# Performance work log

Hardware: AMD Instinct MI355X
Metric: run time of the kernel (lower is better)

The kernel has to match this reference:

```python
import jax, jax.numpy as jnp
import numpy as np

B, C, H, W = 16, 256, 64, 64
OUT_C = 3
N_TOKENS = 512
N_RES = 3
RED = 4
CB = C // RED  # bottleneck channels in ResChain
DN = ('NCHW', 'OIHW', 'NCHW')


def _conv(x, w, pad):
    return jax.lax.conv_general_dilated(x, w, (1, 1), pad, dimension_numbers=DN)


def setup_inputs() -> dict:
    key = jax.random.key(0)
    ks = jax.random.split(key, 8)
    return {
        'input': jax.random.normal(ks[0], (B, C, H, W), jnp.float32),
        'embed': jax.random.normal(ks[1], (C, N_TOKENS), jnp.float32),  # Quantize codebook [dim, n_embed]
        'res_w1': jax.random.normal(ks[2], (N_RES, CB, C, 3, 3), jnp.float32) * 0.02,
        'res_b1': jnp.zeros((N_RES, CB), jnp.float32),
        'res_w2': jax.random.normal(ks[3], (N_RES, C, CB, 1, 1), jnp.float32) * 0.02,
        'res_b2': jnp.zeros((N_RES, C), jnp.float32),
        'out_w': jax.random.normal(ks[4], (OUT_C, C, 1, 1), jnp.float32) * 0.02,
        'out_b': jnp.zeros((OUT_C,), jnp.float32),
    }


def reference(input, embed, res_w1, res_b1, res_w2, res_b2, out_w, out_b):
    sg = jax.lax.stop_gradient
    # --- Quantize (VQ-VAE codebook lookup, straight-through) ---
    x = jnp.transpose(input, (0, 2, 3, 1))  # [B,H,W,C]
    flat = x.reshape(-1, C)                  # [N, C]
    # squared L2 distance to each code: ||f||^2 - 2 f.e + ||e||^2
    dist = (flat * flat).sum(-1, keepdims=True) - 2.0 * (flat @ embed) + (embed * embed).sum(0)
    idx = jnp.argmin(dist, axis=-1).reshape(B, H, W)        # [B,H,W] int
    quantize = jnp.take(embed.T, idx, axis=0)               # embed_code: [B,H,W,C]
    diff = jnp.mean((sg(quantize) - x) ** 2)
    quantize = x + sg(quantize - x)                         # straight-through
    q = jnp.transpose(quantize, (0, 3, 1, 2))               # [B,C,H,W]
    # --- dec: ResChain(n_res_block) + 1x1 conv ---
    for i in range(N_RES):
        h = jax.nn.relu(q)
        h = _conv(h, res_w1[i], 'SAME') + res_b1[i][None, :, None, None]
        h = jax.nn.relu(h)
        h = _conv(h, res_w2[i], 'VALID') + res_b2[i][None, :, None, None]
        q = q + h
    quant = _conv(q, out_w, 'VALID') + out_b[None, :, None, None]  # [B,OUT_C,H,W]
    # --- wordfreq: per-batch bincount over idx (no grad) ---
    flat_idx = idx.reshape(B, -1)
    seg = (flat_idx + jnp.arange(B, dtype=flat_idx.dtype)[:, None] * N_TOKENS).reshape(-1)
    counts = jax.ops.segment_sum(jnp.ones_like(seg, jnp.float32), seg, num_segments=B * N_TOKENS)
    wordfreq = counts.reshape(B, N_TOKENS) / float(H * W)
    return quant, diff.reshape(1), wordfreq
```

## Files before the change

### kernel.cpp

```cpp
#include <hip/hip_runtime.h>


typedef __attribute__((ext_vector_type(8))) short short8;
typedef __attribute__((ext_vector_type(16))) float f32x16;
typedef __attribute__((ext_vector_type(8))) _Float16 half8;
typedef __attribute__((ext_vector_type(2))) _Float16 half2_t;
typedef unsigned short ushort_t;
typedef unsigned long long u64;

#define WS_QA    0
#define WS_QB    8388608
#define WS_ET    16777216
#define WS_EN    16842752
#define WS_EPK   16843264
#define WS_W1PK  16908800
#define WS_W2PK  17129984
#define WS_DIFF  17154560
#define WS_TOK   17154568
#define WS_DST   17220104
#define WS_FN    17285640
#define WS_WL    17351176

#define MARGIN 0.12f

__device__ inline ushort_t f2bf(float f) {
  unsigned u = __float_as_uint(f);
  return (ushort_t)((u + 0x7fffu + ((u >> 16) & 1u)) >> 16);
}
__device__ inline float bf2f(ushort_t h) { return __uint_as_float(((unsigned)h) << 16); }
union HU { _Float16 h; ushort_t u; };
union S8H { short8 s; half8 h; half2_t h2[4]; };

__global__ __launch_bounds__(256) void prep_kernel(
    const float* __restrict__ embed, const float* __restrict__ w1,
    const float* __restrict__ w2, float* __restrict__ ws, float* __restrict__ wf) {
  int i = blockIdx.x * 256 + threadIdx.x;
  if (i < 131072) {
    int t = i >> 8, c = i & 255;
    ((ushort_t*)(ws + WS_ET))[i] = f2bf(embed[c * 512 + t]);
  }
  if (i < 512) {
    float s = 0.f;
    for (int c = 0; c < 256; ++c) { float v = embed[c * 512 + i]; s += v * v; }
    ws[WS_EN + i] = s;
  }
  if (i < 131072) {
    int j = i & 7, lane = (i >> 3) & 63, at = (i >> 9) & 15, ks = i >> 13;
    int code = at * 32 + (lane & 31);
    int c = ks * 16 + (lane >> 5) * 8 + j;
    HU cv; cv.h = (_Float16)embed[c * 512 + code];
    ((ushort_t*)(ws + WS_EPK))[i] = cv.u;
  }
  if (i < 442368) {
    int j = i & 7; int lane = (i >> 3) & 63; int of = (i >> 9) & 1;
    int k16 = (i >> 10) & 15; int rest = i >> 14;
    int tap = rest % 9; int layer = rest / 9;
    int oc = of * 32 + (lane & 31);
    int c = k16 * 16 + (lane >> 5) * 8 + j;
    ((ushort_t*)(ws + WS_W1PK))[i] = f2bf(w1[((layer * 64 + oc) * 256 + c) * 9 + tap]);
  }
  if (i < 49152) {
    int j = i & 7, lane = (i >> 3) & 63, at = (i >> 9) & 7, ks = (i >> 12) & 3, l = i >> 14;
    int co = at * 32 + (lane & 31), cb = ks * 16 + (lane >> 5) * 8 + j;
    ((ushort_t*)(ws + WS_W2PK))[i] = f2bf(w2[(l * 256 + co) * 64 + cb]);
  }
  if (i < 8192) wf[i] = 0.f;
  if (i == 0) { ws[WS_DIFF] = 0.f; ((int*)(ws + WS_WL))[0] = 0; }
}

__global__ __launch_bounds__(512, 4) void dist_kernel(
    const float* __restrict__ input, const half8* __restrict__ epk,
    const float* __restrict__ enorm, int* __restrict__ tok,
    float* __restrict__ dst, float* __restrict__ fnv, int* __restrict__ wl) {
  __shared__ __align__(16) ushort_t sfp[2048 * 8];
  __shared__ float senorm[512];
  __shared__ float trim1[512], trim2[512];
  __shared__ int   trii[512];

  int blk = blockIdx.x, b = blk >> 6, hw0 = (blk & 63) << 6;
  int tid = threadIdx.x, lane = tid & 63, wave = tid >> 6;
  senorm[tid] = enorm[tid];

  {
    int cg = tid >> 3, sub = tid & 7;
    int ks_s = cg >> 2, hi_s = (cg >> 1) & 1, jq = cg & 1;
    const float* src0 = input + ((size_t)(b * 256 + cg * 4)) * 4096 + hw0 + sub * 8;
    float vv[4][8];
#pragma unroll
    for (int m = 0; m < 4; ++m) {
      const float4* s4 = (const float4*)(src0 + (size_t)m * 4096);
      float4 aa = s4[0], bb = s4[1];
      vv[m][0] = aa.x; vv[m][1] = aa.y; vv[m][2] = aa.z; vv[m][3] = aa.w;
      vv[m][4] = bb.x; vv[m][5] = bb.y; vv[m][6] = bb.z; vv[m][7] = bb.w;
    }
    u64* sfp64 = (u64*)sfp;
#pragma unroll
    for (int i = 0; i < 8; ++i) {
      int pl = sub * 8 + i;
      int bt = pl >> 5, lw = (pl & 31) + 32 * hi_s;
      u64 pk = 0;
#pragma unroll
      for (int m = 0; m < 4; ++m) {
        HU cv; cv.h = (_Float16)vv[m][i];
        pk |= ((u64)cv.u) << (16 * m);
      }
      sfp64[((bt * 16 + ks_s) * 64 + lw) * 2 + jq] = pk;
    }
  }
  __syncthreads();

  f32x16 acc[2][2];
#pragma unroll
  for (int bt = 0; bt < 2; ++bt)
#pragma unroll
    for (int a = 0; a < 2; ++a)
#pragma unroll
      for (int r = 0; r < 16; ++r) acc[bt][a][r] = 0.f;

  const short8* sfp8 = (const short8*)sfp;
  float fnp0 = 0.f, fnp1 = 0.f;
#pragma unroll 2
  for (int ks = 0; ks < 16; ++ks) {
    S8H u0, u1;
    u0.s = sfp8[ks * 64 + lane];
    u1.s = sfp8[(16 + ks) * 64 + lane];
#if __has_builtin(__builtin_amdgcn_fdot2)
#pragma unroll
    for (int k = 0; k < 4; ++k) {
      fnp0 = __builtin_amdgcn_fdot2(u0.h2[k], u0.h2[k], fnp0, false);
      fnp1 = __builtin_amdgcn_fdot2(u1.h2[k], u1.h2[k], fnp1, false);
    }
#else
#pragma unroll
    for (int k = 0; k < 8; ++k) {
      float v0 = (float)u0.h[k], v1 = (float)u1.h[k];
      fnp0 += v0 * v0; fnp1 += v1 * v1;
    }
#endif
#pragma unroll
    for (int a = 0; a < 2; ++a) {
      half8 ah = epk[(ks * 16 + wave * 2 + a) * 64 + lane];
      acc[0][a] = __builtin_amdgcn_mfma_f32_32x32x16_f16(ah, u0.h, acc[0][a], 0, 0, 0);
      acc[1][a] = __builtin_amdgcn_mfma_f32_32x32x16_f16(ah, u1.h, acc[1][a], 0, 0, 0);
    }
  }
  fnp0 += __shfl_xor(fnp0, 32, 64);
  fnp1 += __shfl_xor(fnp1, 32, 64);

  int hi5 = lane >> 5;
#pragma unroll
  for (int bt = 0; bt < 2; ++bt) {
    float m1 = 3.4e38f, m2 = 3.4e38f; int i1 = 0;
#pragma unroll
    for (int a = 0; a < 2; ++a)
#pragma unroll
      for (int r = 0; r < 16; ++r) {
        int code = (wave * 2 + a) * 32 + (r & 3) + 8 * (r >> 2) + 4 * hi5;
        float v = senorm[code] - 2.0f * acc[bt][a][r];
        if (v < m1) { m2 = m1; m1 = v; i1 = code; }
        else if (v < m2) m2 = v;
      }
    float o1 = __shfl_xor(m1, 32, 64);
    float o2 = __shfl_xor(m2, 32, 64);
    int   oi = __shfl_xor(i1, 32, 64);
    float n2 = fminf(fmaxf(m1, o1), fminf(m2, o2));
    float n1 = fminf(m1, o1);
    int   ni = (o1 < m1) ? oi : i1;
    if (lane < 32) {
      int p = bt * 32 + lane;
      trim1[p * 8 + wave] = n1; trim2[p * 8 + wave] = n2; trii[p * 8 + wave] = ni;
    }
  }
  __syncthreads();

  if (wave == 0) {
    int p = lane;
    float m1 = trim1[p * 8], m2 = trim2[p * 8]; int i1 = trii[p * 8];
#pragma unroll
    for (int w = 1; w < 8; ++w) {
      float a1 = trim1[p * 8 + w], a2 = trim2[p * 8 + w]; int ai = trii[p * 8 + w];
      float n2 = fminf(fmaxf(m1, a1), fminf(m2, a2));
      if (a1 < m1) { m1 = a1; i1 = ai; }
      m2 = n2;
    }
    float myfn = (lane < 32) ? fnp0 : fnp1;
    int gpos = blk * 64 + p;
    tok[gpos] = i1;
    dst[gpos] = myfn + m1;
    fnv[gpos] = myfn;
    bool flag = (m2 - m1 < MARGIN);
    u64 mk = __ballot(flag);
    int base = 0;
    if (lane == 0 && mk) base = atomicAdd(wl, (int)__popcll(mk));
    base = __shfl(base, 0, 64);
    if (flag) {
      int off = (int)__popcll(mk & ((1ull << lane) - 1ull));
      wl[1 + base + off] = gpos;
    }
  }
}

__global__ __launch_bounds__(256) void redo_kernel(
    const float* __restrict__ input, const float* __restrict__ embed,
    const float* __restrict__ enorm, const int* __restrict__ wl,
    int* __restrict__ tok, float* __restrict__ dst, const float* __restrict__ fnv) {
  __shared__ float sf[256], rv[256];
  __shared__ int   ri[256];
  int n = wl[0];
  int tid = threadIdx.x;
  for (int e = blockIdx.x; e < n; e += gridDim.x) {
    int gpos = wl[1 + e];
    int b = gpos >> 12, hw = gpos & 4095;
    sf[tid] = input[((size_t)(b * 256 + tid)) * 4096 + hw];
    __syncthreads();
    float d0 = 0.f, d1 = 0.f;
#pragma unroll 4
    for (int c = 0; c < 256; ++c) {
      float fv = sf[c];
      d0 += fv * embed[c * 512 + tid];
      d1 += fv * embed[c * 512 + 256 + tid];
    }
    float v0 = enorm[tid] - 2.f * d0;
    float v1 = enorm[256 + tid] - 2.f * d1;
    float bv; int bi;
    if (v1 < v0) { bv = v1; bi = 256 + tid; } else { bv = v0; bi = tid; }
    rv[tid] = bv; ri[tid] = bi;
    __syncthreads();
    for (int s = 128; s > 0; s >>= 1) {
      if (tid < s) {
        float ov = rv[tid + s]; int oi2 = ri[tid + s];
        if (ov < rv[tid] || (ov == rv[tid] && oi2 < ri[tid])) { rv[tid] = ov; ri[tid] = oi2; }
      }
      __syncthreads();
    }
    if (tid == 0) { tok[gpos] = ri[0]; dst[gpos] = fnv[gpos] + rv[0]; }
    __syncthreads();
  }
}

__global__ __launch_bounds__(256) void finalize_kernel(
    const int* __restrict__ tok, const float* __restrict__ dst,
    const ushort_t* __restrict__ embedT, float* __restrict__ wf,
    float* __restrict__ diffp, ushort_t* __restrict__ qout) {
  int blk = blockIdx.x;
  int tid = threadIdx.x, lane = tid & 63, wave = tid >> 6;
  int gbase = blk * 64;
  int b = gbase >> 12;
  if (wave == 0) {
    int t = tok[gbase + lane];
    atomicAdd(&wf[b * 512 + t], 1.0f / 4096.0f);
    float d = dst[gbase + lane];
#pragma unroll
    for (int off = 32; off >= 1; off >>= 1) d += __shfl_down(d, off, 64);
    if (lane == 0) atomicAdd(diffp, d);
  }
#pragma unroll 1
  for (int j = 0; j < 16; ++j) {
    int p = wave * 16 + j;
    int t = __builtin_amdgcn_readfirstlane(tok[gbase + p]);
    const u64* src = (const u64*)(embedT + (size_t)t * 256);
    u64* dstp = (u64*)(qout + ((size_t)(gbase + p)) * 256);
    dstp[lane] = src[lane];
  }
}

__global__ __launch_bounds__(256, 4) void fused_layer(
    const ushort_t* __restrict__ qin, ushort_t* __restrict__ qout,
    const ushort_t* __restrict__ w1pk, const float* __restrict__ b1,
    const ushort_t* __restrict__ w2pk, const float* __restrict__ b2, int l) {
  __shared__ __align__(16) char arena[37888];
  short8*   stg    = (short8*)arena;
  ushort_t* qstage = (ushort_t*)arena;
  ushort_t* hbuf   = (ushort_t*)(arena + 18432);
  float*    sb2    = (float*)(arena + 36864);

  int blk = blockIdx.x;
  int b = blk >> 5; int t = blk & 31;
  int ty0 = (t >> 2) << 3;
  int tx0 = (t & 3) << 4;
  int tid = threadIdx.x, lane = tid & 63, w = tid >> 6;
  int pxh = w & 1, oh = w >> 1;
  int xl = lane & 15, ybit = (lane >> 4) & 1, kb = lane >> 5;

  sb2[tid] = b2[l * 256 + tid];

  f32x16 acc[2];
#pragma unroll
  for (int f = 0; f < 2; ++f)
#pragma unroll
    for (int r = 0; r < 16; ++r) acc[f][r] = 0.f;

  const short8* wp = (const short8*)w1pk + (size_t)l * 18432;
  const short8* w2p = (const short8*)w2pk;

#pragma unroll 1
  for (int cs = 0; cs < 8; ++cs) {
    __syncthreads();
#pragma unroll
    for (int e = 0; e < 3; ++e) {
      int u = e * 256 + tid;
      if (u < 720) {
        int cg = u & 3; int p = u >> 2; int yy = p / 18; int xx = p - yy * 18;
        int sy = ty0 + yy - 1, sx = tx0 + xx - 1;
        short8 sv;
        if (sy >= 0 && sy < 64 && sx >= 0 && sx < 64) {
          sv = *(const short8*)(qin + ((size_t)(b * 4096 + sy * 64 + sx)) * 256 + cs * 32 + cg * 8);
#pragma unroll
          for (int k2 = 0; k2 < 8; ++k2) if (sv[k2] < 0) sv[k2] = 0;
        } else {
#pragma unroll
          for (int k2 = 0; k2 < 8; ++k2) sv[k2] = 0;
        }
        stg[(yy * 4 + cg) * 18 + xx] = sv;
      }
    }
    __syncthreads();
#pragma unroll 1
    for (int dy = 0; dy < 3; ++dy) {
#pragma unroll 1
      for (int dx = 0; dx < 3; ++dx) {
        int tap = dy * 3 + dx;
#pragma unroll
        for (int ks2 = 0; ks2 < 2; ++ks2) {
          int a0i = ((4 * pxh + ybit + dy) * 4 + ks2 * 2 + kb) * 18 + xl + dx;
          short8 A0 = stg[a0i];
          short8 A1 = stg[a0i + 144];
          int k16 = cs * 2 + ks2;
          short8 B = wp[(tap * 16 + k16) * 128 + oh * 64 + lane];
          acc[0] = __builtin_amdgcn_mfma_f32_32x32x16_bf16(A0, B, acc[0], 0, 0, 0);
          acc[1] = __builtin_amdgcn_mfma_f32_32x32x16_bf16(A1, B, acc[1], 0, 0, 0);
        }
      }
    }
  }
  __syncthreads();

  {
    int oc = oh * 32 + (lane & 31);
    float bb = b1[l * 64 + oc];
#pragma unroll
    for (int f = 0; f < 2; ++f)
#pragma unroll
      for (int r = 0; r < 16; ++r) {
        int row = (r & 3) + 8 * (r >> 2) + 4 * kb;
        int pos = (4 * pxh + 2 * f + (row >> 4)) * 16 + (row & 15);
        hbuf[pos * 72 + oc] = f2bf(fmaxf(acc[f][r] + bb, 0.f));
      }
  }
  __syncthreads();

#pragma unroll 1
  for (int qt = 0; qt < 4; ++qt) {
    f32x16 a2[2];
#pragma unroll
    for (int a = 0; a < 2; ++a)
#pragma unroll
      for (int r = 0; r < 16; ++r) a2[a][r] = 0.f;
#pragma unroll
    for (int ks = 0; ks < 4; ++ks) {
      short8 bfr = *(const short8*)(hbuf + (w * 32 + (lane & 31)) * 72 + ks * 16 + kb * 8);
#pragma unroll
      for (int a = 0; a < 2; ++a) {
        short8 afr = w2p[((l * 4 + ks) * 8 + qt * 2 + a) * 64 + lane];
        a2[a] = __builtin_amdgcn_mfma_f32_32x32x16_bf16(afr, bfr, a2[a], 0, 0, 0);
      }
    }
    int pos = w * 32 + (lane & 31);
#pragma unroll
    for (int a = 0; a < 2; ++a)
#pragma unroll
      for (int g = 0; g < 4; ++g) {
        int cob = a * 32 + g * 8 + 4 * kb;
        u64 pk = 0;
#pragma unroll
        for (int k2 = 0; k2 < 4; ++k2) {
          float v = a2[a][g * 4 + k2] + sb2[qt * 64 + cob + k2];
          pk |= ((u64)f2bf(v)) << (16 * k2);
        }
        *(u64*)(qstage + pos * 72 + cob) = pk;
      }
    __syncthreads();
#pragma unroll
    for (int it = 0; it < 4; ++it) {
      int u = it * 256 + tid;
      int px = u >> 3, c8 = u & 7;
      short8 hv = *(const short8*)(qstage + px * 72 + c8 * 8);
      size_t gidx = ((size_t)(b * 4096 + (ty0 + (px >> 4)) * 64 + tx0 + (px & 15))) * 256
                    + qt * 64 + c8 * 8;
      short8 qv = *(const short8*)(qin + gidx);
      short8 ov;
#pragma unroll
      for (int k2 = 0; k2 < 8; ++k2)
        ov[k2] = (short)f2bf(bf2f((ushort_t)qv[k2]) + bf2f((ushort_t)hv[k2]));
      *(short8*)(qout + gidx) = ov;
    }
    __syncthreads();
  }
}

__global__ __launch_bounds__(256) void final_kernel(
    const ushort_t* __restrict__ qbuf, const float* __restrict__ ow,
    const float* __restrict__ ob, float* __restrict__ out,
    const float* __restrict__ ws) {
  int t = blockIdx.x * 256 + threadIdx.x;
  int pos = t >> 4, c16 = t & 15;
  const ushort_t* qp = qbuf + (size_t)pos * 256 + c16 * 16;
  short8 v0 = *(const short8*)qp;
  short8 v1 = *(const short8*)(qp + 8);
  float a0 = 0.f, a1 = 0.f, a2 = 0.f;
#pragma unroll
  for (int k = 0; k < 16; ++k) {
    float f = bf2f((ushort_t)(k < 8 ? v0[k] : v1[k - 8]));
    int c = c16 * 16 + k;
    a0 += f * ow[c];
    a1 += f * ow[256 + c];
    a2 += f * ow[512 + c];
  }
#pragma unroll
  for (int off = 1; off < 16; off <<= 1) {
    a0 += __shfl_xor(a0, off, 64);
    a1 += __shfl_xor(a1, off, 64);
    a2 += __shfl_xor(a2, off, 64);
  }
  if (c16 == 0) {
    int b = pos >> 12, hw = pos & 4095;
    out[(b * 3 + 0) * 4096 + hw] = a0 + ob[0];
    out[(b * 3 + 1) * 4096 + hw] = a1 + ob[1];
    out[(b * 3 + 2) * 4096 + hw] = a2 + ob[2];
  }
  if (t == 0) out[196608] = ws[WS_DIFF] * (1.0f / 16777216.0f);
}

extern "C" void kernel_launch(void* const* d_in, const int* in_sizes, int n_in,
                              void* d_out, int out_size, void* d_ws, size_t ws_size,
                              hipStream_t stream) {
  (void)in_sizes; (void)n_in; (void)out_size; (void)ws_size;
  const float* input = (const float*)d_in[0];
  const float* embed = (const float*)d_in[1];
  const float* b1 = (const float*)d_in[3];
  const float* b2 = (const float*)d_in[5];
  const float* ow = (const float*)d_in[6];
  const float* ob = (const float*)d_in[7];
  float* ws = (float*)d_ws;
  float* out = (float*)d_out;
  float* wf = out + 196609;

  ushort_t* qA = (ushort_t*)(ws + WS_QA);
  ushort_t* qB = (ushort_t*)(ws + WS_QB);
  const ushort_t* et = (const ushort_t*)(ws + WS_ET);
  const half8* epk = (const half8*)(ws + WS_EPK);
  const ushort_t* w1pk = (const ushort_t*)(ws + WS_W1PK);
  const ushort_t* w2pk = (const ushort_t*)(ws + WS_W2PK);
  int*   tok = (int*)(ws + WS_TOK);
  float* dst = ws + WS_DST;
  float* fnv = ws + WS_FN;
  int*   wl  = (int*)(ws + WS_WL);

  hipLaunchKernelGGL(prep_kernel, dim3(1728), dim3(256), 0, stream,
                     embed, (const float*)d_in[2], (const float*)d_in[4], ws, wf);
  hipLaunchKernelGGL(dist_kernel, dim3(1024), dim3(512), 0, stream,
                     input, epk, ws + WS_EN, tok, dst, fnv, wl);
  hipLaunchKernelGGL(redo_kernel, dim3(1024), dim3(256), 0, stream,
                     input, embed, ws + WS_EN, wl, tok, dst, fnv);
  hipLaunchKernelGGL(finalize_kernel, dim3(1024), dim3(256), 0, stream,
                     tok, dst, et, wf, ws + WS_DIFF, qA);
  hipLaunchKernelGGL(fused_layer, dim3(512), dim3(256), 0, stream,
                     qA, qB, w1pk, b1, w2pk, b2, 0);
  hipLaunchKernelGGL(fused_layer, dim3(512), dim3(256), 0, stream,
                     qB, qA, w1pk, b1, w2pk, b2, 1);
  hipLaunchKernelGGL(fused_layer, dim3(512), dim3(256), 0, stream,
                     qA, qB, w1pk, b1, w2pk, b2, 2);
  hipLaunchKernelGGL(final_kernel, dim3(4096), dim3(256), 0, stream,
                     qB, ow, ob, out, ws);
}
```

Baseline: 248.1 us.

## Shrink fused residual tile to 8x8, double-buffer halo staging, write output directly

The fused residual layer now processes 8x8 pixel tiles instead of 16x8, doubling the grid to 1024 blocks and cutting LDS use so more blocks can be resident. Halo staging for each 32-channel slice is double-buffered, so the next slice's global loads overlap the current slice's MFMAs, and one barrier per slice is removed. The second 1x1 conv computes all 256 output channels at once and writes the residual sum straight from registers with scalar bf16 stores, dropping the LDS output staging and its barriers. The trade-offs are a larger halo overhead per pixel, lower weight reuse per tile, and uncoalesced 2-byte global stores.

```diff
diff --git a/kernel.cpp b/kernel.cpp
--- a/kernel.cpp
+++ b/kernel.cpp
@@ -268,40 +268,31 @@
     const ushort_t* __restrict__ qin, ushort_t* __restrict__ qout,
     const ushort_t* __restrict__ w1pk, const float* __restrict__ b1,
     const ushort_t* __restrict__ w2pk, const float* __restrict__ b2, int l) {
-  __shared__ __align__(16) char arena[37888];
-  short8*   stg    = (short8*)arena;
-  ushort_t* qstage = (ushort_t*)arena;
-  ushort_t* hbuf   = (ushort_t*)(arena + 18432);
-  float*    sb2    = (float*)(arena + 36864);
+  __shared__ __align__(16) char arena[24832];
+  short8*   stg  = (short8*)arena;
+  ushort_t* hbuf = (ushort_t*)(arena + 14080);
+  float*    sb2  = (float*)(arena + 23808);
 
   int blk = blockIdx.x;
-  int b = blk >> 5; int t = blk & 31;
-  int ty0 = (t >> 2) << 3;
-  int tx0 = (t & 3) << 4;
+  int b = blk >> 6; int t = blk & 63;
+  int ty0 = (t >> 3) << 3;
+  int tx0 = (t & 7) << 3;
   int tid = threadIdx.x, lane = tid & 63, w = tid >> 6;
-  int pxh = w & 1, oh = w >> 1;
-  int xl = lane & 15, ybit = (lane >> 4) & 1, kb = lane >> 5;
+  int pt = w & 1, ot = w >> 1;
+  int l31 = lane & 31, kb5 = lane >> 5;
 
   sb2[tid] = b2[l * 256 + tid];
 
-  f32x16 acc[2];
-#pragma unroll
-  for (int f = 0; f < 2; ++f)
-#pragma unroll
-    for (int r = 0; r < 16; ++r) acc[f][r] = 0.f;
-
-  const short8* wp = (const short8*)w1pk + (size_t)l * 18432;
+  const short8* wp  = (const short8*)w1pk + (size_t)l * 18432;
   const short8* w2p = (const short8*)w2pk;
 
-#pragma unroll 1
-  for (int cs = 0; cs < 8; ++cs) {
-    __syncthreads();
-#pragma unroll
-    for (int e = 0; e < 3; ++e) {
+  auto stage = [&](int cs, int buf) {
+#pragma unroll
+    for (int e = 0; e < 2; ++e) {
       int u = e * 256 + tid;
-      if (u < 720) {
-        int cg = u & 3; int p = u >> 2; int yy = p / 18; int xx = p - yy * 18;
-        int sy = ty0 + yy - 1, sx = tx0 + xx - 1;
+      if (u < 400) {
+        int cg = u & 3; int pix = u >> 2; int y = pix / 10; int x = pix - y * 10;
+        int sy = ty0 + y - 1, sx = tx0 + x - 1;
         short8 sv;
         if (sy >= 0 && sy < 64 && sx >= 0 && sx < 64) {
           sv = *(const short8*)(qin + ((size_t)(b * 4096 + sy * 64 + sx)) * 256 + cs * 32 + cg * 8);
@@ -311,10 +302,24 @@
 #pragma unroll
           for (int k2 = 0; k2 < 8; ++k2) sv[k2] = 0;
         }
-        stg[(yy * 4 + cg) * 18 + xx] = sv;
+        stg[buf * 440 + (y * 4 + cg) * 11 + x] = sv;
       }
     }
-    __syncthreads();
+  };
+
+  f32x16 acc;
+#pragma unroll
+  for (int r = 0; r < 16; ++r) acc[r] = 0.f;
+
+  int py0 = pt * 4 + (l31 >> 3);
+  int px0 = lane & 7;
+
+  stage(0, 0);
+  __syncthreads();
+#pragma unroll 1
+  for (int cs = 0; cs < 8; ++cs) {
+    if (cs < 7) stage(cs + 1, (cs + 1) & 1);
+    int buf = cs & 1;
 #pragma unroll 1
     for (int dy = 0; dy < 3; ++dy) {
 #pragma unroll 1
@@ -322,79 +327,56 @@
         int tap = dy * 3 + dx;
 #pragma unroll
         for (int ks2 = 0; ks2 < 2; ++ks2) {
-          int a0i = ((4 * pxh + ybit + dy) * 4 + ks2 * 2 + kb) * 18 + xl + dx;
-          short8 A0 = stg[a0i];
-          short8 A1 = stg[a0i + 144];
-          int k16 = cs * 2 + ks2;
-          short8 B = wp[(tap * 16 + k16) * 128 + oh * 64 + lane];
-          acc[0] = __builtin_amdgcn_mfma_f32_32x32x16_bf16(A0, B, acc[0], 0, 0, 0);
-          acc[1] = __builtin_amdgcn_mfma_f32_32x32x16_bf16(A1, B, acc[1], 0, 0, 0);
+          short8 A = stg[buf * 440 + ((py0 + dy) * 4 + ks2 * 2 + kb5) * 11 + px0 + dx];
+          short8 B = wp[(tap * 16 + cs * 2 + ks2) * 128 + ot * 64 + lane];
+          acc = __builtin_amdgcn_mfma_f32_32x32x16_bf16(A, B, acc, 0, 0, 0);
         }
       }
     }
+    __syncthreads();
+  }
+
+  {
+    int oc = ot * 32 + l31;
+    float bb = b1[l * 64 + oc];
+#pragma unroll
+    for (int r = 0; r < 16; ++r) {
+      int row = (r & 3) + 8 * (r >> 2) + 4 * kb5;
+      hbuf[(pt * 32 + row) * 76 + oc] = f2bf(fmaxf(acc[r] + bb, 0.f));
+    }
   }
   __syncthreads();
 
-  {
-    int oc = oh * 32 + (lane & 31);
-    float bb = b1[l * 64 + oc];
-#pragma unroll
-    for (int f = 0; f < 2; ++f)
-#pragma unroll
-      for (int r = 0; r < 16; ++r) {
-        int row = (r & 3) + 8 * (r >> 2) + 4 * kb;
-        int pos = (4 * pxh + 2 * f + (row >> 4)) * 16 + (row & 15);
-        hbuf[pos * 72 + oc] = f2bf(fmaxf(acc[f][r] + bb, 0.f));
-      }
-  }
-  __syncthreads();
+  int pt2 = w & 1, coh = w >> 1;
+  f32x16 acc2[4];
+#pragma unroll
+  for (int a = 0; a < 4; ++a)
+#pragma unroll
+    for (int r = 0; r < 16; ++r) acc2[a][r] = 0.f;
+
+#pragma unroll
+  for (int ks = 0; ks < 4; ++ks) {
+    short8 A = *(const short8*)(hbuf + (pt2 * 32 + l31) * 76 + ks * 16 + kb5 * 8);
+#pragma unroll
+    for (int a = 0; a < 4; ++a) {
+      short8 B = w2p[((l * 4 + ks) * 8 + coh * 4 + a) * 64 + lane];
+      acc2[a] = __builtin_amdgcn_mfma_f32_32x32x16_bf16(A, B, acc2[a], 0, 0, 0);
+    }
+  }
 
 #pragma unroll 1
-  for (int qt = 0; qt < 4; ++qt) {
-    f32x16 a2[2];
-#pragma unroll
-    for (int a = 0; a < 2; ++a)
-#pragma unroll
-      for (int r = 0; r < 16; ++r) a2[a][r] = 0.f;
-#pragma unroll
-    for (int ks = 0; ks < 4; ++ks) {
-      short8 bfr = *(const short8*)(hbuf + (w * 32 + (lane & 31)) * 72 + ks * 16 + kb * 8);
-#pragma unroll
-      for (int a = 0; a < 2; ++a) {
-        short8 afr = w2p[((l * 4 + ks) * 8 + qt * 2 + a) * 64 + lane];
-        a2[a] = __builtin_amdgcn_mfma_f32_32x32x16_bf16(afr, bfr, a2[a], 0, 0, 0);
-      }
-    }
-    int pos = w * 32 + (lane & 31);
-#pragma unroll
-    for (int a = 0; a < 2; ++a)
-#pragma unroll
-      for (int g = 0; g < 4; ++g) {
-        int cob = a * 32 + g * 8 + 4 * kb;
-        u64 pk = 0;
-#pragma unroll
-        for (int k2 = 0; k2 < 4; ++k2) {
-          float v = a2[a][g * 4 + k2] + sb2[qt * 64 + cob + k2];
-          pk |= ((u64)f2bf(v)) << (16 * k2);
-        }
-        *(u64*)(qstage + pos * 72 + cob) = pk;
-      }
-    __syncthreads();
-#pragma unroll
-    for (int it = 0; it < 4; ++it) {
-      int u = it * 256 + tid;
-      int px = u >> 3, c8 = u & 7;
-      short8 hv = *(const short8*)(qstage + px * 72 + c8 * 8);
-      size_t gidx = ((size_t)(b * 4096 + (ty0 + (px >> 4)) * 64 + tx0 + (px & 15))) * 256
-                    + qt * 64 + c8 * 8;
-      short8 qv = *(const short8*)(qin + gidx);
-      short8 ov;
-#pragma unroll
-      for (int k2 = 0; k2 < 8; ++k2)
-        ov[k2] = (short)f2bf(bf2f((ushort_t)qv[k2]) + bf2f((ushort_t)hv[k2]));
-      *(short8*)(qout + gidx) = ov;
-    }
-    __syncthreads();
+  for (int a = 0; a < 4; ++a) {
+    int co = coh * 128 + a * 32 + l31;
+    float bb2 = sb2[co];
+#pragma unroll
+    for (int r = 0; r < 16; ++r) {
+      int row = (r & 3) + 8 * (r >> 2) + 4 * kb5;
+      int pos = pt2 * 32 + row;
+      int gy = ty0 + (pos >> 3), gx = tx0 + (pos & 7);
+      size_t gidx = ((size_t)(b * 4096 + gy * 64 + gx)) * 256 + co;
+      float v = acc2[a][r] + bb2 + bf2f(qin[gidx]);
+      qout[gidx] = f2bf(v);
+    }
   }
 }
 
@@ -464,11 +446,11 @@
                      input, embed, ws + WS_EN, wl, tok, dst, fnv);
   hipLaunchKernelGGL(finalize_kernel, dim3(1024), dim3(256), 0, stream,
                      tok, dst, et, wf, ws + WS_DIFF, qA);
-  hipLaunchKernelGGL(fused_layer, dim3(512), dim3(256), 0, stream,
+  hipLaunchKernelGGL(fused_layer, dim3(1024), dim3(256), 0, stream,
                      qA, qB, w1pk, b1, w2pk, b2, 0);
-  hipLaunchKernelGGL(fused_layer, dim3(512), dim3(256), 0, stream,
+  hipLaunchKernelGGL(fused_layer, dim3(1024), dim3(256), 0, stream,
                      qB, qA, w1pk, b1, w2pk, b2, 1);
-  hipLaunchKernelGGL(fused_layer, dim3(512), dim3(256), 0, stream,
+  hipLaunchKernelGGL(fused_layer, dim3(1024), dim3(256), 0, stream,
                      qA, qB, w1pk, b1, w2pk, b2, 2);
   hipLaunchKernelGGL(final_kernel, dim3(4096), dim3(256), 0, stream,
                      qB, ow, ob, out, ws);
```

New measurement: 288.2 us. 1.16x slower.
